# Kernel optimization log

Measured on AMD Instinct MI355X. Metric: run time of the kernel, lower is better.

The kernel has to match this reference:

```python
import jax, jax.numpy as jnp
import numpy as np

K = 3
PAD = 1


def bilinear_gather(xr, py, px):
    # xr: [B, G, H, W, C] channels-last per offset group; py/px: [B, G, H, W] sample coords
    B, G, H, W, C = xr.shape
    y0 = jnp.floor(py)
    x0 = jnp.floor(px)
    wy = py - y0
    wx = px - x0
    y0i = y0.astype(jnp.int32)
    x0i = x0.astype(jnp.int32)
    bi = jnp.arange(B)[:, None, None, None]
    gi = jnp.arange(G)[None, :, None, None]
    out = jnp.zeros(py.shape + (C,), xr.dtype)
    corners = (
        (0, 0, (1 - wy) * (1 - wx)),
        (0, 1, (1 - wy) * wx),
        (1, 0, wy * (1 - wx)),
        (1, 1, wy * wx),
    )
    for dy_, dx_, w in corners:
        yy = y0i + dy_
        xx = x0i + dx_
        valid = ((yy >= 0) & (yy < H) & (xx >= 0) & (xx < W)).astype(xr.dtype)
        yc = jnp.clip(yy, 0, H - 1)
        xc = jnp.clip(xx, 0, W - 1)
        v = xr[bi, gi, yc, xc]  # [B,G,H,W,C]
        out = out + (w * valid)[..., None] * v
    return out


def setup_inputs() -> dict:
    key = jax.random.key(0)
    k1, k2, k3, k4, k5 = jax.random.split(key, 5)
    B, Cin, H, W = 4, 64, 256, 256
    G, OC = 8, 64
    KK = K * K
    x = jax.random.normal(k1, (B, Cin, H, W), jnp.float32)
    offset = jax.random.normal(k2, (B, 2, G * KK, H, W), jnp.float32)
    mask = jax.random.normal(k3, (B, G * KK, H, W), jnp.float32)
    weight = jax.random.normal(k4, (OC, Cin // G, K, K), jnp.float32) * 0.05
    bias = jax.random.normal(k5, (OC,), jnp.float32) * 0.01
    return {"x": x, "offset": offset, "mask": mask, "weight": weight, "bias": bias}


def reference(x, offset, mask, weight, bias):
    B, Cin, H, W = x.shape
    OC, Cpg, _, _ = weight.shape
    G = Cin // Cpg          # conv groups == offset groups here
    OPG = OC // G
    KK = K * K
    # replicate module's permute(0,2,1,3,4).flip(1).view(b,-1,fh,fw):
    # pair axis (dy,dx) is input dim 1; combined (group,tap) axis is reversed
    off = jnp.flip(offset, axis=2)                      # [B,2,G*KK,H,W]
    dy = off[:, 0].reshape(B, G, KK, H, W)
    dx = off[:, 1].reshape(B, G, KK, H, W)
    m = jax.nn.sigmoid(mask).reshape(B, G, KK, H, W)
    xr = x.reshape(B, G, Cpg, H, W).transpose(0, 1, 3, 4, 2)  # [B,G,H,W,Cpg]
    wg = weight.reshape(G, OPG, Cpg, K, K)
    iy = jnp.arange(H, dtype=x.dtype)[None, None, :, None]
    ix = jnp.arange(W, dtype=x.dtype)[None, None, None, :]
    out = jnp.zeros((B, G, OPG, H, W), x.dtype)
    for t in range(KK):  # fixed small loop over kernel taps
        ki, kj = t // K, t % K
        py = iy - PAD + ki + dy[:, :, t]
        px = ix - PAD + kj + dx[:, :, t]
        s = bilinear_gather(xr, py, px) * m[:, :, t][..., None]  # [B,G,H,W,Cpg]
        out = out + jnp.einsum('bghwc,gdc->bgdhw', s, wg[:, :, :, ki, kj])
    return out.reshape(B, OC, H, W) + bias[None, :, None, None]
```

## Files before the change

### kernel.cpp

```cpp
#include <hip/hip_runtime.h>
#include <hip/hip_fp16.h>


#define KSZ 3
#define PAD 1

static constexpr int B   = 4;
static constexpr int Cin = 64;
static constexpr int H   = 256;
static constexpr int W   = 256;
static constexpr int G   = 8;
static constexpr int OC  = 64;
static constexpr int KK  = KSZ * KSZ;
static constexpr int Cpg = Cin / G;
static constexpr int OPG = OC / G;
static constexpr int HW  = H * W;
static constexpr int NXCD = 8;

static constexpr int WROWS  = 12;
static constexpr int WUP    = 5;
static constexpr int WPITCH = 257;

typedef _Float16 f16x8  __attribute__((ext_vector_type(8)));
typedef float    f32x16 __attribute__((ext_vector_type(16)));

union U4H {
    uint4 u;
    __half2 h2[4];
    _Float16 h[8];
    f16x8 v;
};

__global__ __launch_bounds__(256) void transpose_kernel(
    const float* __restrict__ x, uint4* __restrict__ xt)
{
    const int h = blockIdx.x, g = blockIdx.y, b = blockIdx.z;
    const int w = threadIdx.x;
    const int pix = h * W + w;
    const float* src = x + (size_t)(b * Cin + g * Cpg) * HW + pix;
    U4H v;
#pragma unroll
    for (int c = 0; c < 8; ++c) v.h[c] = (_Float16)src[(size_t)c * HW];
    xt[(size_t)(b * G + g) * HW + pix] = v.u;
}

__global__ __launch_bounds__(320) void prep_weights(
    const float* __restrict__ weight, uint4* __restrict__ wfrag)
{
    const int g    = blockIdx.x;
    const int tid  = threadIdx.x;
    const int m    = tid >> 6;
    const int lane = tid & 63;
    const int hi   = lane >> 5;
    const int lp   = lane & 31;
    const int t    = 2 * m + hi;
    U4H a;
#pragma unroll
    for (int c = 0; c < 8; ++c) {
        float v = 0.0f;
        if (lp < OPG && t < KK)
            v = weight[((size_t)(g * OPG + lp) * Cpg + c) * KK + t];
        a.h[c] = (_Float16)v;
    }
    wfrag[((size_t)g * 5 + m) * 64 + lane] = a.u;
}

__global__ __launch_bounds__(256, 3) void dcn_kernel(
    const uint4* __restrict__ xt,
    const uint4* __restrict__ wfrag,
    const float* __restrict__ offset,
    const float* __restrict__ mask,
    const float* __restrict__ bias,
    float* __restrict__ out)
{
    __shared__ uint4 win[WROWS * WPITCH];

    const unsigned id = blockIdx.x;
    const unsigned wl = (id & (NXCD - 1)) * (gridDim.x / NXCD) + (id >> 3);
    const int h  = wl & (H - 1);
    const int bg = wl >> 8;
    const int g  = bg & (G - 1);
    const int b  = bg >> 3;

    const int tid  = threadIdx.x;
    const int lane = tid & 63;
    const int wave = tid >> 6;
    const int hi   = lane >> 5;
    const int lp   = lane & 31;

    const uint4* xb = xt + (size_t)(b * G + g) * HW;
    const int h0 = h - WUP;

#pragma unroll
    for (int i = 0; i < WROWS; ++i) {
        const int wr = min(max(h0 + i, 0), H - 1);
        win[i * WPITCH + tid] = xb[wr * W + tid];
    }

    f16x8 afrag[5];
    {
        const uint4* wf = wfrag + (size_t)g * 5 * 64 + lane;
#pragma unroll
        for (int m = 0; m < 5; ++m) {
            U4H tmp; tmp.u = wf[m * 64];
            afrag[m] = tmp.v;
        }
    }

    const float* offy = offset + (size_t)(b * 2 + 0) * (G * KK) * HW;
    const float* offx = offset + (size_t)(b * 2 + 1) * (G * KK) * HW;
    const float* mk   = mask + (size_t)b * (G * KK) * HW;

    float dyv[2][5], dxv[2][5], msv[2][5];
#pragma unroll
    for (int tile = 0; tile < 2; ++tile) {
        const int wq  = wave * 64 + tile * 32 + lp;
        const int pix = h * W + wq;
#pragma unroll
        for (int m = 0; m < 5; ++m) {
            const int t  = 2 * m + hi;
            const int tt = (t > 8) ? 8 : t;
            const int idx0 = G * KK - 1 - (g * KK + tt);
            dyv[tile][m] = offy[(size_t)idx0 * HW + pix];
            dxv[tile][m] = offx[(size_t)idx0 * HW + pix];
            const float mv = mk[(size_t)(g * KK + tt) * HW + pix];
            float s = 1.0f / (1.0f + __expf(-mv));
            msv[tile][m] = (t <= 8) ? s : 0.0f;
        }
    }

    __syncthreads();

    auto sample = [&](int t, int wq, float dy, float dx, float msig) -> f16x8 {
        const int tt = (t > 8) ? 8 : t;
        const int ki = (tt >= 3) + (tt >= 6);
        const int kj = tt - 3 * ki;

        const float py = (float)(h - PAD + ki) + dy;
        const float px = (float)(wq - PAD + kj) + dx;
        const float y0f = floorf(py), x0f = floorf(px);
        const float wy = py - y0f, wx = px - x0f;
        const int y0 = (int)y0f, x0 = (int)x0f;
        const int iy0 = y0 - h0, iy1 = iy0 + 1;

        float w00, w01, w10, w11;
        uint4 v00, v01, v10, v11;

        const bool ok = (y0 >= 0) & (y0 + 1 < H) & (x0 >= 0) & (x0 + 1 < W) &
                        ((unsigned)iy0 <= (unsigned)(WROWS - 2));
        if (__all((int)ok)) {
            const float u = (1.f - wy) * msig, v = wy * msig;
            w00 = u * (1.f - wx); w01 = u * wx;
            w10 = v * (1.f - wx); w11 = v * wx;
            const int a0 = iy0 * WPITCH + x0;
            v00 = win[a0];          v01 = win[a0 + 1];
            v10 = win[a0 + WPITCH]; v11 = win[a0 + WPITCH + 1];
        } else {
            const bool vy0 = (y0 >= 0) & (y0 < H), vy1 = (y0 + 1 >= 0) & (y0 + 1 < H);
            const bool vx0 = (x0 >= 0) & (x0 < W), vx1 = (x0 + 1 >= 0) & (x0 + 1 < W);
            const float u   = vy0 ? (1.f - wy) * msig : 0.f;
            const float v   = vy1 ? wy * msig : 0.f;
            const float cx0 = vx0 ? (1.f - wx) : 0.f;
            const float cx1 = vx1 ? wx : 0.f;
            w00 = u * cx0; w01 = u * cx1; w10 = v * cx0; w11 = v * cx1;

            const int i0 = min(max(iy0, 0), WROWS - 1);
            const int i1 = min(max(iy1, 0), WROWS - 1);
            const int xc0 = min(max(x0, 0), W - 1);
            const int xc1 = min(max(x0 + 1, 0), W - 1);
            v00 = win[i0 * WPITCH + xc0];
            v01 = win[i0 * WPITCH + xc1];
            v10 = win[i1 * WPITCH + xc0];
            v11 = win[i1 * WPITCH + xc1];

            const bool bad = (vy0 & ((unsigned)iy0 > (unsigned)(WROWS - 1))) |
                             (vy1 & ((unsigned)iy1 > (unsigned)(WROWS - 1)));
            if (__builtin_expect(__any((int)bad), 0)) {
                if (bad) {
                    const int yc0 = min(max(y0, 0), H - 1);
                    const int yc1 = min(max(y0 + 1, 0), H - 1);
                    v00 = xb[yc0 * W + xc0];
                    v01 = xb[yc0 * W + xc1];
                    v10 = xb[yc1 * W + xc0];
                    v11 = xb[yc1 * W + xc1];
                }
            }
        }

        U4H a, bq, c, d; a.u = v00; bq.u = v01; c.u = v10; d.u = v11;
        const __half2 hw00 = __float2half2_rn(w00);
        const __half2 hw01 = __float2half2_rn(w01);
        const __half2 hw10 = __float2half2_rn(w10);
        const __half2 hw11 = __float2half2_rn(w11);
        U4H s;
#pragma unroll
        for (int i = 0; i < 4; ++i)
            s.h2[i] = __hfma2(hw00, a.h2[i],
                      __hfma2(hw01, bq.h2[i],
                      __hfma2(hw10, c.h2[i],
                      __hmul2(hw11, d.h2[i]))));
        return s.v;
    };

    f32x16 acc0 = {};
    f32x16 acc1 = {};
    {
        const int wq = wave * 64 + lp;
#pragma unroll
        for (int m = 0; m < 5; ++m)
            acc0 = __builtin_amdgcn_mfma_f32_32x32x16_f16(
                afrag[m], sample(2 * m + hi, wq, dyv[0][m], dxv[0][m], msv[0][m]), acc0, 0, 0, 0);
    }
    {
        const int wq = wave * 64 + 32 + lp;
#pragma unroll
        for (int m = 0; m < 5; ++m)
            acc1 = __builtin_amdgcn_mfma_f32_32x32x16_f16(
                afrag[m], sample(2 * m + hi, wq, dyv[1][m], dxv[1][m], msv[1][m]), acc1, 0, 0, 0);
    }

#pragma unroll
    for (int tile = 0; tile < 2; ++tile) {
        const int wq = wave * 64 + tile * 32 + lp;
#pragma unroll
        for (int r = 0; r < 4; ++r) {
            const int dd = r + 4 * hi;
            const float v = (tile == 0 ? acc0[r] : acc1[r]) + bias[g * OPG + dd];
            out[((size_t)b * OC + g * OPG + dd) * HW + h * W + wq] = v;
        }
    }
}

extern "C" void kernel_launch(void* const* d_in, const int* in_sizes, int n_in,
                              void* d_out, int out_size, void* d_ws, size_t ws_size,
                              hipStream_t stream) {
    const float* x      = (const float*)d_in[0];
    const float* offset = (const float*)d_in[1];
    const float* mask   = (const float*)d_in[2];
    const float* weight = (const float*)d_in[3];
    const float* bias   = (const float*)d_in[4];
    float* out = (float*)d_out;

    uint4* xt    = (uint4*)d_ws;
    uint4* wfrag = (uint4*)((char*)d_ws + (size_t)B * G * HW * 16);

    dim3 tgrid(H, G, B);
    transpose_kernel<<<tgrid, dim3(256), 0, stream>>>(x, xt);
    prep_weights<<<dim3(G), dim3(320), 0, stream>>>(weight, wfrag);
    dcn_kernel<<<dim3(B * G * H), dim3(256), 0, stream>>>(xt, wfrag, offset, mask, bias, out);
}
```

Before: 96.08 us.

## Tile DCN blocks as 4x64 pixel patches with a 2D shared halo window

Each block now covers a 4-row by 64-column patch, with one wave per row, instead of one full image row. It stages a 15x75 halo window in shared memory rather than 12 full rows. This cuts the redundant window loads: the old layout reloaded 12 rows for every output row, while the new one loads about 4.4x the patch area. The cost is more out-of-window fallbacks to global memory at the column edges, integer div/mod in the staging loop, and removal of the occupancy hint from launch_bounds.

```diff
diff --git a/kernel.cpp b/kernel.cpp
--- a/kernel.cpp
+++ b/kernel.cpp
@@ -17,9 +17,12 @@
 static constexpr int HW  = H * W;
 static constexpr int NXCD = 8;
 
-static constexpr int WROWS  = 12;
-static constexpr int WUP    = 5;
-static constexpr int WPITCH = 257;
+static constexpr int BR    = 4;
+static constexpr int BC    = 64;
+static constexpr int MARG  = 5;
+static constexpr int WROWS = BR + 2 * MARG + 1;
+static constexpr int WCOLS = 75;
+static constexpr int WUSED = BC + 2 * MARG;
 
 typedef _Float16 f16x8  __attribute__((ext_vector_type(8)));
 typedef float    f32x16 __attribute__((ext_vector_type(16)));
@@ -65,7 +68,7 @@
     wfrag[((size_t)g * 5 + m) * 64 + lane] = a.u;
 }
 
-__global__ __launch_bounds__(256, 3) void dcn_kernel(
+__global__ __launch_bounds__(256) void dcn_kernel(
     const uint4* __restrict__ xt,
     const uint4* __restrict__ wfrag,
     const float* __restrict__ offset,
@@ -73,14 +76,19 @@
     const float* __restrict__ bias,
     float* __restrict__ out)
 {
-    __shared__ uint4 win[WROWS * WPITCH];
+    __shared__ uint4 win[WROWS * WCOLS];
 
     const unsigned id = blockIdx.x;
     const unsigned wl = (id & (NXCD - 1)) * (gridDim.x / NXCD) + (id >> 3);
-    const int h  = wl & (H - 1);
-    const int bg = wl >> 8;
-    const int g  = bg & (G - 1);
-    const int b  = bg >> 3;
+    const int colblk = wl & 3;
+    const int rowblk = (wl >> 2) & 63;
+    const int g      = (wl >> 8) & (G - 1);
+    const int b      = wl >> 11;
+
+    const int h_base = rowblk * BR;
+    const int xbase  = colblk * BC;
+    const int h0     = h_base - MARG;
+    const int x0base = xbase - MARG;
 
     const int tid  = threadIdx.x;
     const int lane = tid & 63;
@@ -88,13 +96,20 @@
     const int hi   = lane >> 5;
     const int lp   = lane & 31;
 
+    const int h = h_base + wave;
+
     const uint4* xb = xt + (size_t)(b * G + g) * HW;
-    const int h0 = h - WUP;
-
-#pragma unroll
-    for (int i = 0; i < WROWS; ++i) {
-        const int wr = min(max(h0 + i, 0), H - 1);
-        win[i * WPITCH + tid] = xb[wr * W + tid];
+
+#pragma unroll
+    for (int it = 0; it < 5; ++it) {
+        const int k = it * 256 + tid;
+        if (k < WROWS * WCOLS) {
+            const int i = k / WCOLS;
+            const int j = k - i * WCOLS;
+            const int gr = min(max(h0 + i, 0), H - 1);
+            const int gc = min(max(x0base + j, 0), W - 1);
+            win[k] = xb[gr * W + gc];
+        }
     }
 
     f16x8 afrag[5];
@@ -114,7 +129,7 @@
     float dyv[2][5], dxv[2][5], msv[2][5];
 #pragma unroll
     for (int tile = 0; tile < 2; ++tile) {
-        const int wq  = wave * 64 + tile * 32 + lp;
+        const int wq  = xbase + tile * 32 + lp;
         const int pix = h * W + wq;
 #pragma unroll
         for (int m = 0; m < 5; ++m) {
@@ -141,20 +156,22 @@
         const float y0f = floorf(py), x0f = floorf(px);
         const float wy = py - y0f, wx = px - x0f;
         const int y0 = (int)y0f, x0 = (int)x0f;
-        const int iy0 = y0 - h0, iy1 = iy0 + 1;
+        const int iy0 = y0 - h0;
+        const int ix0 = x0 - x0base;
 
         float w00, w01, w10, w11;
         uint4 v00, v01, v10, v11;
 
         const bool ok = (y0 >= 0) & (y0 + 1 < H) & (x0 >= 0) & (x0 + 1 < W) &
-                        ((unsigned)iy0 <= (unsigned)(WROWS - 2));
+                        ((unsigned)iy0 <= (unsigned)(WROWS - 2)) &
+                        ((unsigned)ix0 <= (unsigned)(WUSED - 2));
         if (__all((int)ok)) {
             const float u = (1.f - wy) * msig, v = wy * msig;
             w00 = u * (1.f - wx); w01 = u * wx;
             w10 = v * (1.f - wx); w11 = v * wx;
-            const int a0 = iy0 * WPITCH + x0;
-            v00 = win[a0];          v01 = win[a0 + 1];
-            v10 = win[a0 + WPITCH]; v11 = win[a0 + WPITCH + 1];
+            const int a0 = iy0 * WCOLS + ix0;
+            v00 = win[a0];         v01 = win[a0 + 1];
+            v10 = win[a0 + WCOLS]; v11 = win[a0 + WCOLS + 1];
         } else {
             const bool vy0 = (y0 >= 0) & (y0 < H), vy1 = (y0 + 1 >= 0) & (y0 + 1 < H);
             const bool vx0 = (x0 >= 0) & (x0 < W), vx1 = (x0 + 1 >= 0) & (x0 + 1 < W);
@@ -164,21 +181,26 @@
             const float cx1 = vx1 ? wx : 0.f;
             w00 = u * cx0; w01 = u * cx1; w10 = v * cx0; w11 = v * cx1;
 
-            const int i0 = min(max(iy0, 0), WROWS - 1);
-            const int i1 = min(max(iy1, 0), WROWS - 1);
-            const int xc0 = min(max(x0, 0), W - 1);
-            const int xc1 = min(max(x0 + 1, 0), W - 1);
-            v00 = win[i0 * WPITCH + xc0];
-            v01 = win[i0 * WPITCH + xc1];
-            v10 = win[i1 * WPITCH + xc0];
-            v11 = win[i1 * WPITCH + xc1];
-
-            const bool bad = (vy0 & ((unsigned)iy0 > (unsigned)(WROWS - 1))) |
-                             (vy1 & ((unsigned)iy1 > (unsigned)(WROWS - 1)));
+            const int i0  = min(max(iy0, 0), WROWS - 1);
+            const int i1  = min(max(iy0 + 1, 0), WROWS - 1);
+            const int jx0 = min(max(ix0, 0), WUSED - 1);
+            const int jx1 = min(max(ix0 + 1, 0), WUSED - 1);
+            v00 = win[i0 * WCOLS + jx0];
+            v01 = win[i0 * WCOLS + jx1];
+            v10 = win[i1 * WCOLS + jx0];
+            v11 = win[i1 * WCOLS + jx1];
+
+            const bool bad =
+                (vy0 & ((unsigned)iy0 > (unsigned)(WROWS - 1))) |
+                (vy1 & ((unsigned)(iy0 + 1) > (unsigned)(WROWS - 1))) |
+                (vx0 & ((unsigned)ix0 > (unsigned)(WUSED - 1))) |
+                (vx1 & ((unsigned)(ix0 + 1) > (unsigned)(WUSED - 1)));
             if (__builtin_expect(__any((int)bad), 0)) {
                 if (bad) {
                     const int yc0 = min(max(y0, 0), H - 1);
                     const int yc1 = min(max(y0 + 1, 0), H - 1);
+                    const int xc0 = min(max(x0, 0), W - 1);
+                    const int xc1 = min(max(x0 + 1, 0), W - 1);
                     v00 = xb[yc0 * W + xc0];
                     v01 = xb[yc0 * W + xc1];
                     v10 = xb[yc1 * W + xc0];
@@ -205,14 +227,14 @@
     f32x16 acc0 = {};
     f32x16 acc1 = {};
     {
-        const int wq = wave * 64 + lp;
+        const int wq = xbase + lp;
 #pragma unroll
         for (int m = 0; m < 5; ++m)
             acc0 = __builtin_amdgcn_mfma_f32_32x32x16_f16(
                 afrag[m], sample(2 * m + hi, wq, dyv[0][m], dxv[0][m], msv[0][m]), acc0, 0, 0, 0);
     }
     {
-        const int wq = wave * 64 + 32 + lp;
+        const int wq = xbase + 32 + lp;
 #pragma unroll
         for (int m = 0; m < 5; ++m)
             acc1 = __builtin_amdgcn_mfma_f32_32x32x16_f16(
@@ -221,7 +243,7 @@
 
 #pragma unroll
     for (int tile = 0; tile < 2; ++tile) {
-        const int wq = wave * 64 + tile * 32 + lp;
+        const int wq = xbase + tile * 32 + lp;
 #pragma unroll
         for (int r = 0; r < 4; ++r) {
             const int dd = r + 4 * hi;
@@ -247,5 +269,6 @@
     dim3 tgrid(H, G, B);
     transpose_kernel<<<tgrid, dim3(256), 0, stream>>>(x, xt);
     prep_weights<<<dim3(G), dim3(320), 0, stream>>>(weight, wfrag);
-    dcn_kernel<<<dim3(B * G * H), dim3(256), 0, stream>>>(xt, wfrag, offset, mask, bias, out);
-}
+    dcn_kernel<<<dim3(B * G * (H / BR) * (W / BC)), dim3(256), 0, stream>>>(
+        xt, wfrag, offset, mask, bias, out);
+}
```

Result: slower. 98.19 us (+2.2%).
